# Optimization experiments

Measured on AMD Instinct MI355X. Metric: run time of the kernel, lower is better.

Reference implementation:

```python
import jax, jax.numpy as jnp
import numpy as np

THRESHOLD1 = 1.0
THRESHOLD2 = 1.0


def _conv(x, w, stride, pad):
    return jax.lax.conv_general_dilated(
        x, w, window_strides=(stride, stride),
        padding=((pad, pad), (pad, pad)),
        dimension_numbers=('NCHW', 'OIHW', 'NCHW'))


def _percentiles_1_to_99(t):
    # Faithful to torch: k = 1 + round(0.01*q*(n-1)); kthvalue = k-th smallest.
    # One sort + static gather replaces 99 kthvalue calls.
    flat = jnp.sort(t.reshape(-1))
    n = flat.shape[0]  # static under jit
    ks = np.array([1 + round(0.01 * q * (n - 1)) for q in range(1, 100)], dtype=np.int64)
    return flat[ks - 1]  # [99]


def setup_inputs() -> dict:
    key = jax.random.key(0)
    k1, k2, k3, k4 = jax.random.split(key, 4)
    x = jax.random.normal(k1, (64, 128, 56, 56), jnp.float32)
    # Kaiming-ish scaled conv weights
    w1 = jax.random.normal(k2, (256, 128, 3, 3), jnp.float32) * (2.0 / (128 * 9)) ** 0.5
    w2 = jax.random.normal(k3, (256, 256, 3, 3), jnp.float32) * (2.0 / (256 * 9)) ** 0.5
    w_id = jax.random.normal(k4, (256, 128, 1, 1), jnp.float32) * (2.0 / 128) ** 0.5
    return {"x": x, "w1": w1, "w2": w2, "w_id": w_id}


def reference(x, w1, w2, w_id):
    out1 = _conv(x, w1, 2, 1)                 # conv1: [64,256,28,28]
    a = _percentiles_1_to_99(out1)            # percentiles of UNclamped conv1 output
    out = jnp.clip(out1, 0.0, THRESHOLD1)     # out[out>t1]=t1; out[out<0]=0
    # dropout(p=0.0 / eval) is identity
    out = _conv(out, w2, 1, 1)                # conv2
    out = out + _conv(x, w_id, 2, 0)          # residual via 1x1 stride-2 downsample
    b = _percentiles_1_to_99(out)             # percentiles before second clamp
    out = jnp.clip(out, 0.0, THRESHOLD2)
    return out, a, b
```

## Files before the change

### kernel.cpp

```cpp
#include <hip/hip_runtime.h>

typedef unsigned short ushort_t;
typedef unsigned int uint_t;

using short8 = __attribute__((ext_vector_type(8))) short;
using f32x4  = __attribute__((ext_vector_type(4))) float;

#define N_BATCH   64
#define C_MID     256
#define H_OUT     28
#define W_OUT     28
#define SPATIAL   (H_OUT*W_OUT)
#define OUT_ELEMS (N_BATCH*C_MID*SPATIAL)

#define NBINS 2048
#define BIN_LO (-16.0f)
#define BIN_INV 64.0f
#define BIN_W  0.015625f

#define XT_ROW   (57*128)
#define XT_IMG   (57*57*128)
#define O1_ROW   (30*256)
#define O1_IMG   (30*30*256)

__device__ __forceinline__ ushort_t f2bf(float f) {
    uint_t u = __float_as_uint(f);
    u += 0x7FFFu + ((u >> 16) & 1u);
    return (ushort_t)(u >> 16);
}

__device__ __forceinline__ void gll16(const ushort_t* g, void* l) {
    __builtin_amdgcn_global_load_lds(
        (const __attribute__((address_space(1))) unsigned int*)g,
        (__attribute__((address_space(3))) unsigned int*)l, 16, 0, 0);
}

__global__ __launch_bounds__(256) void zwtrans(
    uint_t* __restrict__ xT32, uint_t* __restrict__ o1T32,
    const float* __restrict__ w1, const float* __restrict__ w2,
    const float* __restrict__ wid, ushort_t* __restrict__ wT1,
    ushort_t* __restrict__ wT2)
{
    const int bxx = blockIdx.x, y = blockIdx.y, tid = threadIdx.x;
    if (bxx < 87) {
        int i = bxx * 256 + tid;
        int n = y;
        if (i >= 22080) return;
        if (i < 7232) {
            uint_t* base = xT32 + (size_t)n * (XT_IMG / 2);
            if (i < 3648) base[i] = 0;
            else { int j = i - 3648; int r = (j >> 6) + 1;
                   base[r * (XT_ROW / 2) + (j & 63)] = 0; }
        } else {
            int k = i - 7232;
            uint_t* base = o1T32 + (size_t)n * (O1_IMG / 2);
            if (k < 3840) base[k] = 0;
            else if (k < 7680) base[29 * (O1_ROW / 2) + (k - 3840)] = 0;
            else if (k < 11264) { int j = k - 7680; int r = (j >> 7) + 1;
                   base[r * (O1_ROW / 2) + (j & 127)] = 0; }
            else { int j = k - 11264; int r = (j >> 7) + 1;
                   base[r * (O1_ROW / 2) + 29 * 128 + (j & 127)] = 0; }
        }
    } else {
        int idx = ((bxx - 87) * 64 + y) * 256 + tid;
        if (idx < 256 * 1152) {
            int co = idx / 1152, k = idx % 1152;
            int g = k >> 7, ci = k & 127;
            wT1[idx] = f2bf(w1[(co * 128 + ci) * 9 + g]);
        }
        if (idx < 256 * 2432) {
            int co = idx / 2432, k = idx % 2432;
            float v;
            if (k < 2304) { int g = k >> 8, ci = k & 255; v = w2[(co * 256 + ci) * 9 + g]; }
            else          { v = wid[co * 128 + (k - 2304)]; }
            wT2[idx] = f2bf(v);
        }
    }
}

__global__ __launch_bounds__(256) void xtrans(
    const float* __restrict__ x, ushort_t* __restrict__ xT)
{
    __shared__ ushort_t t[224 * 130];
    const int tid = threadIdx.x;
    const int g = blockIdx.x, n = blockIdx.y;
    const float* xs = x + ((size_t)n * 128) * 3136 + g * 4 * 56;

    for (int it = 0; it < 112; ++it) {
        int f = it * 256 + tid;
        int ci = f / 224, rem = f % 224;
        t[rem * 130 + ci] = f2bf(xs[ci * 3136 + rem]);
    }
    __syncthreads();
    ushort_t* xo = xT + (size_t)n * XT_IMG + (g * 4 + 1) * XT_ROW + 128;
    for (int it = 0; it < 56; ++it) {
        int f = it * 256 + tid;
        int pos = f >> 6, c2 = f & 63;
        int r = pos / 56, iw = pos % 56;
        uint_t v = *(const uint_t*)&t[pos * 130 + c2 * 2];
        *(uint_t*)(xo + r * XT_ROW + iw * 128 + c2 * 2) = v;
    }
}

__global__ __launch_bounds__(256, 2) void conv1_mfma(
    const ushort_t* __restrict__ xT, const ushort_t* __restrict__ wT1,
    ushort_t* __restrict__ o1T, ushort_t* __restrict__ bh)
{
    const int bx = blockIdx.x;
    const int tid = threadIdx.x;
    const int wv = tid >> 6, lane = tid & 63;
    const int ln = lane & 15, quad = lane >> 4;
    const int n = bx / 7, rg = bx % 7, r0 = rg * 4;

    __shared__ short8 Ald[2 * 1024];
    __shared__ short8 Bp[2304];

    f32x4 acc[4][7];
    #pragma unroll
    for (int a = 0; a < 4; ++a)
        #pragma unroll
        for (int b = 0; b < 7; ++b) acc[a][b] = (f32x4){0.f, 0.f, 0.f, 0.f};

    int drb[7], cl0[7];
    #pragma unroll
    for (int b = 0; b < 7; ++b) {
        int p = b * 16 + ln;
        drb[b] = 2 * (p / 28);
        cl0[b] = p % 28;
    }

    uint_t poff[9];
    #pragma unroll
    for (int i = 0; i < 9; ++i) {
        int slot = (i * 4 + wv) * 64 + lane;
        int s2 = min(slot, 2051);
        int k8 = s2 / 513;
        int rem = s2 - k8 * 513;
        int dr = rem / 57, j = rem - dr * 57;
        int col = (j < 29) ? (2 * j) : (2 * (j - 29) + 1);
        poff[i] = (uint_t)((2 * r0 + dr) * XT_ROW + col * 128 + k8 * 8);
    }
    const uint_t aoff = (uint_t)((wv * 64 + lane) * 1152);

    const ushort_t* xTimg = xT + (size_t)n * XT_IMG;

    auto stageA = [&](int tap, int c, int buf) {
        #pragma unroll
        for (int jj = 0; jj < 4; ++jj)
            gll16(wT1 + aoff + jj * 8 + tap * 128 + c * 32,
                  (char*)Ald + buf * 16384 + (jj * 256 + wv * 64) * 16);
    };

    for (int c = 0; c < 4; ++c) {
        #pragma unroll
        for (int i = 0; i < 9; ++i)
            gll16(xTimg + poff[i] + c * 32, (char*)Bp + ((i * 4 + wv) * 64) * 16);
        if (c == 0) stageA(0, 0, 0);
        __syncthreads();

        for (int t = 0; t < 9; ++t) {
            const int st = c * 9 + t;
            const int buf = st & 1;
            if (t < 8)      stageA(t + 1, c, buf ^ 1);
            else if (c < 3) stageA(0, c + 1, buf ^ 1);
            const int kh = t / 3, kw = t - kh * 3;
            short8 af[4], bf[7];
            #pragma unroll
            for (int a = 0; a < 4; ++a)
                af[a] = Ald[buf * 1024 + quad * 256 + wv * 64 + a * 16 + ln];
            #pragma unroll
            for (int b = 0; b < 7; ++b) {
                int dr = drb[b] + kh;
                int j = (kw == 1) ? (29 + cl0[b]) : (cl0[b] + (kw >> 1));
                bf[b] = Bp[quad * 513 + dr * 57 + j];
            }
            #pragma unroll
            for (int a = 0; a < 4; ++a)
                #pragma unroll
                for (int b = 0; b < 7; ++b)
                    acc[a][b] = __builtin_amdgcn_mfma_f32_16x16x32_bf16(
                        af[a], bf[b], acc[a][b], 0, 0, 0);
            __syncthreads();
        }
    }

    uint_t* hist = (uint_t*)Ald;
    for (int i = tid; i < NBINS; i += 256) hist[i] = 0;
    __syncthreads();

    ushort_t* oimg = o1T + (size_t)n * O1_IMG;
    #pragma unroll
    for (int a = 0; a < 4; ++a) {
        int co = wv * 64 + a * 16 + quad * 4;
        #pragma unroll
        for (int b = 0; b < 7; ++b) {
            int p = b * 16 + ln;
            int h = r0 + p / 28, w = p % 28;
            ushort_t pk[4];
            #pragma unroll
            for (int r = 0; r < 4; ++r) {
                float v = acc[a][b][r];
                int bin = (int)((v - BIN_LO) * BIN_INV);
                bin = min(max(bin, 0), NBINS - 1);
                atomicAdd(&hist[bin], 1u);
                pk[r] = f2bf(fminf(fmaxf(v, 0.f), 1.f));
            }
            uint2 u; u.x = (uint_t)pk[0] | ((uint_t)pk[1] << 16);
            u.y = (uint_t)pk[2] | ((uint_t)pk[3] << 16);
            *(uint2*)(oimg + ((h + 1) * 30 + (w + 1)) * 256 + co) = u;
        }
    }

    __syncthreads();
    size_t blin = (size_t)bx * NBINS;
    for (int i = tid; i < NBINS; i += 256) bh[blin + i] = (ushort_t)hist[i];
}

__global__ __launch_bounds__(256, 2) void conv2_mfma(
    const ushort_t* __restrict__ o1T, const ushort_t* __restrict__ xT,
    const ushort_t* __restrict__ wT2, float* __restrict__ fout,
    ushort_t* __restrict__ bh)
{
    const int bx = blockIdx.x;
    const int by = blockIdx.y;
    const int tid = threadIdx.x;
    const int wv = tid >> 6, lane = tid & 63;
    const int ln = lane & 15, quad = lane >> 4;
    const int n = bx >> 2, rg = bx & 3, r0 = rg * 8;
    const int coh = wv & 1;
    const int pt  = wv >> 1;

    __shared__ short8 Ad[2 * 1024];
    __shared__ short8 Bp[2560];

    f32x4 acc[4][7];
    #pragma unroll
    for (int a = 0; a < 4; ++a)
        #pragma unroll
        for (int b = 0; b < 7; ++b) acc[a][b] = (f32x4){0.f, 0.f, 0.f, 0.f};

    int prb[7], cl0[7], hlog[7];
    #pragma unroll
    for (int b = 0; b < 7; ++b) {
        int p = b * 16 + ln;
        int h = r0 + pt * 4 + p / 28;
        hlog[b] = h;
        prb[b] = (min(h, 27) - r0) * 32;
        cl0[b] = p % 28;
    }

    uint_t po[10];
    #pragma unroll
    for (int jj = 0; jj < 10; ++jj) {
        int f = (wv * 10 + jj) * 64 + lane;
        int ci8 = f / 320, rem = f % 320;
        int dr = rem >> 5, cl = rem & 31;
        po[jj] = (uint_t)(min(r0 + dr, 29) * O1_ROW + cl * 256 + ci8 * 8);
    }
    uint_t io[7];
    #pragma unroll
    for (int jj = 0; jj < 7; ++jj) {
        int f = (wv * 7 + jj) * 64 + lane;
        int ci8 = f / 224, pos = f % 224;
        int h = min(r0 + pos / 28, 27), w = pos % 28;
        io[jj] = (uint_t)(((2 * h + 1) * 57 + (2 * w + 1)) * 128 + ci8 * 8);
    }

    const ushort_t* Abase = wT2 + (size_t)(by * 128 + lane) * 2432;
    const ushort_t* o1img = o1T + (size_t)n * O1_IMG;
    const ushort_t* xTimg = xT + (size_t)n * XT_IMG;

    auto stageA = [&](int k0, int buf) {
        #pragma unroll
        for (int j = 0; j < 4; ++j)
            gll16(Abase + (j & 1) * 64 * 2432 + (wv * 2 + (j >> 1)) * 8 + k0,
                  (char*)Ad + buf * 16384 + (wv * 4 + j) * 1024);
    };

    for (int c = 0; c < 4; ++c) {
        #pragma unroll
        for (int jj = 0; jj < 10; ++jj)
            gll16(o1img + po[jj] + c * 64, (char*)Bp + (wv * 10 + jj) * 1024);
        if (c == 0) stageA(0, 0);
        __syncthreads();

        for (int t = 0; t < 9; ++t) {
            const int as = c * 9 + t;
            if (t < 8)      stageA((t + 1) * 256 + c * 64, (as + 1) & 1);
            else if (c < 3) stageA(c * 64 + 64, (as + 1) & 1);
            else            stageA(2304, (as + 1) & 1);
            const int ab = (as & 1) * 1024;
            const int kh = t / 3, kw = t - kh * 3;
            #pragma unroll
            for (int kk = 0; kk < 2; ++kk) {
                short8 af[4], bf[7];
                #pragma unroll
                for (int a = 0; a < 4; ++a)
                    af[a] = Ad[ab + (kk * 4 + quad) * 128 + coh * 64 + a * 16 + ln];
                #pragma unroll
                for (int b = 0; b < 7; ++b)
                    bf[b] = Bp[(kk * 4 + quad) * 320 + prb[b] + kh * 32 + cl0[b] + kw];
                #pragma unroll
                for (int a = 0; a < 4; ++a)
                    #pragma unroll
                    for (int b = 0; b < 7; ++b)
                        acc[a][b] = __builtin_amdgcn_mfma_f32_16x16x32_bf16(
                            af[a], bf[b], acc[a][b], 0, 0, 0);
            }
            __syncthreads();
        }
    }

    for (int cid = 0; cid < 2; ++cid) {
        #pragma unroll
        for (int jj = 0; jj < 7; ++jj)
            gll16(xTimg + io[jj] + cid * 64, (char*)Bp + (wv * 7 + jj) * 1024);
        __syncthreads();
        if (cid == 0) stageA(2368, 1);
        const int ab = ((36 + cid) & 1) * 1024;
        #pragma unroll
        for (int kk = 0; kk < 2; ++kk) {
            short8 af[4], bf[7];
            #pragma unroll
            for (int a = 0; a < 4; ++a)
                af[a] = Ad[ab + (kk * 4 + quad) * 128 + coh * 64 + a * 16 + ln];
            #pragma unroll
            for (int b = 0; b < 7; ++b)
                bf[b] = Bp[(kk * 4 + quad) * 224 + pt * 112 + b * 16 + ln];
            #pragma unroll
            for (int a = 0; a < 4; ++a)
                #pragma unroll
                for (int b = 0; b < 7; ++b)
                    acc[a][b] = __builtin_amdgcn_mfma_f32_16x16x32_bf16(
                        af[a], bf[b], acc[a][b], 0, 0, 0);
        }
        __syncthreads();
    }

    uint_t* hist = (uint_t*)Ad;
    for (int i = tid; i < NBINS; i += 256) hist[i] = 0;
    __syncthreads();

    #pragma unroll
    for (int a = 0; a < 4; ++a) {
        int co = by * 128 + coh * 64 + a * 16 + quad * 4;
        #pragma unroll
        for (int b = 0; b < 7; ++b) {
            if (hlog[b] <= 27) {
                #pragma unroll
                for (int r = 0; r < 4; ++r) {
                    float v = acc[a][b][r];
                    int bin = (int)((v - BIN_LO) * BIN_INV);
                    bin = min(max(bin, 0), NBINS - 1);
                    atomicAdd(&hist[bin], 1u);
                    fout[((size_t)(n * 256 + co + r)) * SPATIAL +
                         hlog[b] * 28 + cl0[b]] = fminf(fmaxf(v, 0.f), 1.f);
                }
            }
        }
    }

    __syncthreads();
    size_t blin = (size_t)(by * 256 + bx) * NBINS;
    for (int i = tid; i < NBINS; i += 256) bh[blin + i] = (ushort_t)hist[i];
}

__global__ __launch_bounds__(256) void hreduce(
    const ushort_t* __restrict__ bh, uint_t* __restrict__ hf, int nblk)
{
    __shared__ uint_t p[256];
    int b0 = blockIdx.x * 64;
    int binl = threadIdx.x & 63, grp = threadIdx.x >> 6;
    uint_t s = 0;
    for (int j = grp; j < nblk; j += 4) s += bh[(size_t)j * NBINS + b0 + binl];
    p[threadIdx.x] = s;
    __syncthreads();
    if (threadIdx.x < 64)
        hf[b0 + threadIdx.x] = p[threadIdx.x] + p[64 + threadIdx.x] +
                               p[128 + threadIdx.x] + p[192 + threadIdx.x];
}

__global__ __launch_bounds__(1024) void select_k(
    const uint_t* __restrict__ hf, float* __restrict__ outp)
{
    __shared__ uint_t cs[1024];
    int t = threadIdx.x;
    uint_t s = hf[2 * t] + hf[2 * t + 1];
    cs[t] = s;
    __syncthreads();
    for (int d = 1; d < 1024; d <<= 1) {
        uint_t v = (t >= d) ? cs[t - d] : 0;
        __syncthreads();
        cs[t] += v;
        __syncthreads();
    }
    if (t >= 1 && t <= 99) {
        long long k = 1 + (long long)llrint(0.01 * (double)t * (double)(OUT_ELEMS - 1));
        int lo = 0, hi = 1023;
        while (lo < hi) { int mid = (lo + hi) >> 1; if ((long long)cs[mid] < k) lo = mid + 1; else hi = mid; }
        long long cum = (lo == 0) ? 0 : (long long)cs[lo - 1];
        int b = lo * 2;
        while (cum + (long long)hf[b] < k) { cum += hf[b]; ++b; }
        outp[t - 1] = BIN_LO + ((float)b + 0.5f) * BIN_W;
    }
}

extern "C" void kernel_launch(void* const* d_in, const int* in_sizes, int n_in,
                              void* d_out, int out_size, void* d_ws, size_t ws_size,
                              hipStream_t stream)
{
    const float* x   = (const float*)d_in[0];
    const float* w1  = (const float*)d_in[1];
    const float* w2  = (const float*)d_in[2];
    const float* wid = (const float*)d_in[3];
    float* out = (float*)d_out;

    char* ws = (char*)d_ws;
    ushort_t* xT  = (ushort_t*)ws;
    ushort_t* o1T = (ushort_t*)(ws + 53235712);
    ushort_t* wT1 = (ushort_t*)(ws + 82731008);
    ushort_t* wT2 = (ushort_t*)(ws + 83320832);
    ushort_t* bhA = (ushort_t*)(ws + 84566016);
    ushort_t* bhB = (ushort_t*)(ws + 86401024);
    uint_t*   hfA = (uint_t*)  (ws + 88498176);
    uint_t*   hfB = (uint_t*)  (ws + 88506368);

    zwtrans<<<dim3(125, 64), 256, 0, stream>>>((uint_t*)xT, (uint_t*)o1T,
                                               w1, w2, wid, wT1, wT2);
    xtrans<<<dim3(14, 64), 256, 0, stream>>>(x, xT);

    conv1_mfma<<<448, 256, 0, stream>>>(xT, wT1, o1T, bhA);
    conv2_mfma<<<dim3(256, 2), 256, 0, stream>>>(o1T, xT, wT2, out, bhB);

    hreduce<<<32, 256, 0, stream>>>(bhA, hfA, 448);
    select_k<<<1, 1024, 0, stream>>>(hfA, out + OUT_ELEMS);
    hreduce<<<32, 256, 0, stream>>>(bhB, hfB, 512);
    select_k<<<1, 1024, 0, stream>>>(hfB, out + OUT_ELEMS + 99);
}
```

Measured before the change: 406.0 us.

## Software-pipeline conv kernels with vmcnt waits, triple-buffered weights and double-buffered inputs

```diff
diff --git a/kernel.cpp b/kernel.cpp
--- a/kernel.cpp
+++ b/kernel.cpp
@@ -22,6 +22,9 @@
 #define XT_IMG   (57*57*128)
 #define O1_ROW   (30*256)
 #define O1_IMG   (30*30*256)
+
+#define WAITVM(n) asm volatile("s_waitcnt vmcnt(" #n ")" ::: "memory")
+#define BARRIER() asm volatile("s_barrier" ::: "memory")
 
 __device__ __forceinline__ ushort_t f2bf(float f) {
     uint_t u = __float_as_uint(f);
@@ -152,17 +155,21 @@
     };
 
     for (int c = 0; c < 4; ++c) {
+        BARRIER();
         #pragma unroll
         for (int i = 0; i < 9; ++i)
             gll16(xTimg + poff[i] + c * 32, (char*)Bp + ((i * 4 + wv) * 64) * 16);
         if (c == 0) stageA(0, 0, 0);
-        __syncthreads();
-
+        WAITVM(0);
+        BARRIER();
+
+        #pragma unroll
         for (int t = 0; t < 9; ++t) {
             const int st = c * 9 + t;
             const int buf = st & 1;
             if (t < 8)      stageA(t + 1, c, buf ^ 1);
             else if (c < 3) stageA(0, c + 1, buf ^ 1);
+            if (c == 3 && t == 8) { WAITVM(0); } else { WAITVM(4); }
             const int kh = t / 3, kw = t - kh * 3;
             short8 af[4], bf[7];
             #pragma unroll
@@ -174,16 +181,18 @@
                 int j = (kw == 1) ? (29 + cl0[b]) : (cl0[b] + (kw >> 1));
                 bf[b] = Bp[quad * 513 + dr * 57 + j];
             }
+            __builtin_amdgcn_s_setprio(1);
             #pragma unroll
             for (int a = 0; a < 4; ++a)
                 #pragma unroll
                 for (int b = 0; b < 7; ++b)
                     acc[a][b] = __builtin_amdgcn_mfma_f32_16x16x32_bf16(
                         af[a], bf[b], acc[a][b], 0, 0, 0);
-            __syncthreads();
-        }
-    }
-
+            __builtin_amdgcn_s_setprio(0);
+        }
+    }
+
+    __syncthreads();
     uint_t* hist = (uint_t*)Ald;
     for (int i = tid; i < NBINS; i += 256) hist[i] = 0;
     __syncthreads();
@@ -230,8 +239,8 @@
     const int coh = wv & 1;
     const int pt  = wv >> 1;
 
-    __shared__ short8 Ad[2 * 1024];
-    __shared__ short8 Bp[2560];
+    __shared__ short8 Ad[3 * 512];
+    __shared__ short8 Bp[2 * 1280];
 
     f32x4 acc[4][7];
     #pragma unroll
@@ -249,94 +258,106 @@
         cl0[b] = p % 28;
     }
 
-    uint_t po[10];
-    #pragma unroll
-    for (int jj = 0; jj < 10; ++jj) {
-        int f = (wv * 10 + jj) * 64 + lane;
+    uint_t po[5];
+    #pragma unroll
+    for (int jj = 0; jj < 5; ++jj) {
+        int f = (wv * 5 + jj) * 64 + lane;
         int ci8 = f / 320, rem = f % 320;
         int dr = rem >> 5, cl = rem & 31;
         po[jj] = (uint_t)(min(r0 + dr, 29) * O1_ROW + cl * 256 + ci8 * 8);
     }
-    uint_t io[7];
-    #pragma unroll
-    for (int jj = 0; jj < 7; ++jj) {
-        int f = (wv * 7 + jj) * 64 + lane;
-        int ci8 = f / 224, pos = f % 224;
+    uint_t io[4];
+    #pragma unroll
+    for (int jj = 0; jj < 4; ++jj) {
+        int i2 = min(wv * 4 + jj, 13);
+        int slot = i2 * 64 + lane;
+        int ci8 = slot / 224, pos = slot % 224;
         int h = min(r0 + pos / 28, 27), w = pos % 28;
         io[jj] = (uint_t)(((2 * h + 1) * 57 + (2 * w + 1)) * 128 + ci8 * 8);
     }
 
-    const ushort_t* Abase = wT2 + (size_t)(by * 128 + lane) * 2432;
     const ushort_t* o1img = o1T + (size_t)n * O1_IMG;
     const ushort_t* xTimg = xT + (size_t)n * XT_IMG;
+    const ushort_t* Ab0 = wT2 + (size_t)(by * 128 + lane) * 2432 + wv * 8;
+    const ushort_t* Ab1 = Ab0 + (size_t)64 * 2432;
 
     auto stageA = [&](int k0, int buf) {
-        #pragma unroll
-        for (int j = 0; j < 4; ++j)
-            gll16(Abase + (j & 1) * 64 * 2432 + (wv * 2 + (j >> 1)) * 8 + k0,
-                  (char*)Ad + buf * 16384 + (wv * 4 + j) * 1024);
+        gll16(Ab0 + k0, (char*)Ad + buf * 8192 + wv * 2048);
+        gll16(Ab1 + k0, (char*)Ad + buf * 8192 + wv * 2048 + 1024);
     };
-
-    for (int c = 0; c < 4; ++c) {
-        #pragma unroll
-        for (int jj = 0; jj < 10; ++jj)
-            gll16(o1img + po[jj] + c * 64, (char*)Bp + (wv * 10 + jj) * 1024);
-        if (c == 0) stageA(0, 0);
-        __syncthreads();
-
+    auto stageB = [&](int hb, int coff) {
+        #pragma unroll
+        for (int jj = 0; jj < 5; ++jj)
+            gll16(o1img + po[jj] + coff, (char*)Bp + hb * 20480 + (wv * 5 + jj) * 1024);
+    };
+    auto stageI = [&](int ib, int idh) {
+        #pragma unroll
+        for (int jj = 0; jj < 4; ++jj) {
+            int i2 = min(wv * 4 + jj, 13);
+            gll16(xTimg + io[jj] + idh * 32, (char*)Bp + ib * 20480 + i2 * 1024);
+        }
+    };
+
+    stageB(0, 0);
+    stageA(0, 0);
+
+    for (int h = 0; h < 8; ++h) {
+        #pragma unroll
         for (int t = 0; t < 9; ++t) {
-            const int as = c * 9 + t;
-            if (t < 8)      stageA((t + 1) * 256 + c * 64, (as + 1) & 1);
-            else if (c < 3) stageA(c * 64 + 64, (as + 1) & 1);
-            else            stageA(2304, (as + 1) & 1);
-            const int ab = (as & 1) * 1024;
+            if (t < 8)      stageA((t + 1) * 256 + h * 32, (t + 1) % 3);
+            else if (h < 7) stageA((h + 1) * 32, 0);
+            else            stageA(2304, 0);
+            if (t == 1) {
+                if (h < 7) { stageB((h + 1) & 1, (h + 1) * 32); WAITVM(7); }
+                else       { stageI(0, 0);                      WAITVM(6); }
+            } else {
+                WAITVM(2);
+            }
+            BARRIER();
+            const int abuf = t % 3;
             const int kh = t / 3, kw = t - kh * 3;
-            #pragma unroll
-            for (int kk = 0; kk < 2; ++kk) {
-                short8 af[4], bf[7];
-                #pragma unroll
-                for (int a = 0; a < 4; ++a)
-                    af[a] = Ad[ab + (kk * 4 + quad) * 128 + coh * 64 + a * 16 + ln];
-                #pragma unroll
-                for (int b = 0; b < 7; ++b)
-                    bf[b] = Bp[(kk * 4 + quad) * 320 + prb[b] + kh * 32 + cl0[b] + kw];
-                #pragma unroll
-                for (int a = 0; a < 4; ++a)
-                    #pragma unroll
-                    for (int b = 0; b < 7; ++b)
-                        acc[a][b] = __builtin_amdgcn_mfma_f32_16x16x32_bf16(
-                            af[a], bf[b], acc[a][b], 0, 0, 0);
-            }
-            __syncthreads();
-        }
-    }
-
-    for (int cid = 0; cid < 2; ++cid) {
-        #pragma unroll
-        for (int jj = 0; jj < 7; ++jj)
-            gll16(xTimg + io[jj] + cid * 64, (char*)Bp + (wv * 7 + jj) * 1024);
-        __syncthreads();
-        if (cid == 0) stageA(2368, 1);
-        const int ab = ((36 + cid) & 1) * 1024;
-        #pragma unroll
-        for (int kk = 0; kk < 2; ++kk) {
             short8 af[4], bf[7];
             #pragma unroll
             for (int a = 0; a < 4; ++a)
-                af[a] = Ad[ab + (kk * 4 + quad) * 128 + coh * 64 + a * 16 + ln];
+                af[a] = Ad[abuf * 512 + quad * 128 + coh * 64 + a * 16 + ln];
             #pragma unroll
             for (int b = 0; b < 7; ++b)
-                bf[b] = Bp[(kk * 4 + quad) * 224 + pt * 112 + b * 16 + ln];
+                bf[b] = Bp[(h & 1) * 1280 + quad * 320 + prb[b] + kh * 32 + cl0[b] + kw];
+            __builtin_amdgcn_s_setprio(1);
             #pragma unroll
             for (int a = 0; a < 4; ++a)
                 #pragma unroll
                 for (int b = 0; b < 7; ++b)
                     acc[a][b] = __builtin_amdgcn_mfma_f32_16x16x32_bf16(
                         af[a], bf[b], acc[a][b], 0, 0, 0);
-        }
-        __syncthreads();
-    }
-
+            __builtin_amdgcn_s_setprio(0);
+        }
+    }
+
+    #pragma unroll
+    for (int idh = 0; idh < 4; ++idh) {
+        if (idh < 3) { stageA(2304 + (idh + 1) * 32, (idh + 1) % 3); WAITVM(2); }
+        else         { WAITVM(0); }
+        BARRIER();
+        if (idh < 3) stageI((idh + 1) & 1, idh + 1);
+        short8 af[4], bf[7];
+        #pragma unroll
+        for (int a = 0; a < 4; ++a)
+            af[a] = Ad[(idh % 3) * 512 + quad * 128 + coh * 64 + a * 16 + ln];
+        #pragma unroll
+        for (int b = 0; b < 7; ++b)
+            bf[b] = Bp[(idh & 1) * 1280 + quad * 224 + pt * 112 + b * 16 + ln];
+        __builtin_amdgcn_s_setprio(1);
+        #pragma unroll
+        for (int a = 0; a < 4; ++a)
+            #pragma unroll
+            for (int b = 0; b < 7; ++b)
+                acc[a][b] = __builtin_amdgcn_mfma_f32_16x16x32_bf16(
+                    af[a], bf[b], acc[a][b], 0, 0, 0);
+        __builtin_amdgcn_s_setprio(0);
+    }
+
+    __syncthreads();
     uint_t* hist = (uint_t*)Ad;
     for (int i = tid; i < NBINS; i += 256) hist[i] = 0;
     __syncthreads();
```

Measured after the change: 393.4 us. -3.1%, faster.
